# Kernel tuning notes

Measured on AMD Instinct MI355X. Metric: run time of the kernel, lower is better.

Reference implementation:

```python
import jax, jax.numpy as jnp
import numpy as np

D_IN = 4097   # 4096 obj feat + 1 depth
D_H1 = 512
D_H2 = 256
N_HEADS = 4
D_HEAD = D_H2 // N_HEADS
D_FF = 512


def setup_inputs() -> dict:
    key = jax.random.key(0)
    ks = jax.random.split(key, 20)
    B, T, N = 2, 100, 30
    s = lambda *sh: 1.0 / np.sqrt(sh[0])
    inp = {
        "object_features": jax.random.normal(ks[0], (B, T, N, 4096), jnp.float32),
        "object_depths": jax.random.uniform(ks[1], (B, T, N, 1), jnp.float32),
        # spatial encoder (2-layer fully-connected message passing)
        "W1a": jax.random.normal(ks[2], (D_IN, D_H1), jnp.float32) * s(D_IN),
        "W2a": jax.random.normal(ks[3], (D_IN, D_H1), jnp.float32) * s(D_IN),
        "b1a": jnp.zeros((D_H1,), jnp.float32),
        "W1b": jax.random.normal(ks[4], (D_H1, D_H2), jnp.float32) * s(D_H1),
        "W2b": jax.random.normal(ks[5], (D_H1, D_H2), jnp.float32) * s(D_H1),
        "b1b": jnp.zeros((D_H2,), jnp.float32),
        # temporal transformer encoder layer (post-LN)
        "Wq": jax.random.normal(ks[6], (D_H2, D_H2), jnp.float32) * s(D_H2),
        "Wk": jax.random.normal(ks[7], (D_H2, D_H2), jnp.float32) * s(D_H2),
        "Wv": jax.random.normal(ks[8], (D_H2, D_H2), jnp.float32) * s(D_H2),
        "Wo": jax.random.normal(ks[9], (D_H2, D_H2), jnp.float32) * s(D_H2),
        "ln1_g": jnp.ones((D_H2,), jnp.float32),
        "ln1_b": jnp.zeros((D_H2,), jnp.float32),
        "Wf1": jax.random.normal(ks[10], (D_H2, D_FF), jnp.float32) * s(D_H2),
        "bf1": jnp.zeros((D_FF,), jnp.float32),
        "Wf2": jax.random.normal(ks[11], (D_FF, D_H2), jnp.float32) * s(D_FF),
        "bf2": jnp.zeros((D_H2,), jnp.float32),
        "ln2_g": jnp.ones((D_H2,), jnp.float32),
        "ln2_b": jnp.zeros((D_H2,), jnp.float32),
        # classifier
        "Wc": jax.random.normal(ks[12], (D_H2, 1), jnp.float32) * s(D_H2),
        "bc": jnp.zeros((1,), jnp.float32),
    }
    return inp


def _layer_norm(x, g, b, eps=1e-5):
    mu = jnp.mean(x, axis=-1, keepdims=True)
    var = jnp.var(x, axis=-1, keepdims=True)
    return (x - mu) * jax.lax.rsqrt(var + eps) * g + b


def _forward(object_features, object_depths, W1a, W2a, b1a, W1b, W2b, b1b,
             Wq, Wk, Wv, Wo, ln1_g, ln1_b, Wf1, bf1, Wf2, bf2, ln2_g, ln2_b,
             Wc, bc):
    B, T, N, _ = object_features.shape
    x = jnp.concatenate([object_features, object_depths], axis=-1)  # (B,T,N,4097)
    # fully-connected graph (torch.combinations, both directions):
    # aggregated message for node i = mean over all j != i.
    def mp(h, Ws, Wn, b):
        neigh = (jnp.sum(h, axis=2, keepdims=True) - h) / (N - 1)
        return jax.nn.relu(h @ Ws + neigh @ Wn + b)
    h = mp(x, W1a, W2a, b1a)      # (B,T,N,512)
    h = mp(h, W1b, W2b, b1b)      # (B,T,N,256)
    g = jnp.mean(h, axis=2)       # global mean pool -> (B,T,256)
    # temporal transformer encoder (self-attention over T, post-LN)
    q = (g @ Wq).reshape(B, T, N_HEADS, D_HEAD)
    k = (g @ Wk).reshape(B, T, N_HEADS, D_HEAD)
    v = (g @ Wv).reshape(B, T, N_HEADS, D_HEAD)
    scores = jnp.einsum("bthd,bshd->bhts", q, k) / np.sqrt(D_HEAD)
    attn = jax.nn.softmax(scores, axis=-1)
    ctx = jnp.einsum("bhts,bshd->bthd", attn, v).reshape(B, T, D_H2) @ Wo
    y = _layer_norm(g + ctx, ln1_g, ln1_b)
    ff = jax.nn.relu(y @ Wf1 + bf1) @ Wf2 + bf2
    z = _layer_norm(y + ff, ln2_g, ln2_b)  # (B,T,256)
    # dropout is identity in eval mode -> probs2 == probs, uncertainty == 0
    logits = (z @ Wc + bc).squeeze(-1)     # (B,T)
    probs = jax.nn.sigmoid(logits)
    uncertainty = jnp.zeros_like(probs)
    return probs, uncertainty


def reference(object_features, object_depths, W1a, W2a, b1a, W1b, W2b, b1b,
              Wq, Wk, Wv, Wo, ln1_g, ln1_b, Wf1, bf1, Wf2, bf2, ln2_g, ln2_b,
              Wc, bc):
    return _forward(object_features, object_depths, W1a, W2a, b1a, W1b, W2b,
                    b1b, Wq, Wk, Wv, Wo, ln1_g, ln1_b, Wf1, bf1, Wf2, bf2,
                    ln2_g, ln2_b, Wc, bc)
```

## Files before the change

### kernel.cpp

```cpp
#include <hip/hip_runtime.h>
#include <hip/hip_bf16.h>
#include <stdint.h>

typedef unsigned short u16;
typedef __attribute__((ext_vector_type(8))) short short8;
typedef __attribute__((ext_vector_type(4))) float floatx4;
typedef __attribute__((ext_vector_type(4))) unsigned short ushort4_t;

#define BT 200
#define NOBJ 30
#define KP2 4224
#define DIN 4097
#define DH1 512
#define DH2 256
#define DFF 512
#define MPAD 6016
#define CHZ 176
#define NBIGW (132*16)
#define NSMALL 512
#define NCONV (BT*2)
#define NPAD 13
#define NZERO 16

#define PSTR1 ((size_t)6000 * DH1)
#define PSTR2 ((size_t)6000 * DH2)

__device__ __forceinline__ u16 f2bf(float f) {
    union { float f; uint32_t u; } c; c.f = f;
    uint32_t u = c.u;
    u += 0x7FFF + ((u >> 16) & 1);
    return (u16)(u >> 16);
}

__device__ __forceinline__ void load16_lds(const u16* g, u16* l) {
    __builtin_amdgcn_global_load_lds(
        (const __attribute__((address_space(1))) void*)g,
        (__attribute__((address_space(3))) void*)l, 16, 0, 0);
}

__device__ __forceinline__ size_t tile_off(int ytile, int row, int c8) {
    int z = c8 / CHZ, rem = c8 - z * CHZ;
    int i = rem >> 3, kw = rem & 7;
    int ks = kw ^ (row & 7);
    return ((((size_t)(ytile * 3 + z) * 22 + i) * 128 + row) * 64) + ks * 8;
}

__global__ __launch_bounds__(256, 4)
void prep_all(const float* __restrict__ W1a, const float* __restrict__ W2a,
              const float* __restrict__ W1b, const float* __restrict__ W2b,
              const float* __restrict__ feat, const float* __restrict__ depth,
              u16* __restrict__ Wc1T, u16* __restrict__ W2aTs,
              u16* __restrict__ Wc2T, u16* __restrict__ W2bTs,
              u16* __restrict__ XbT, u16* __restrict__ SbT,
              float* __restrict__ zeroBase, size_t zeroQuads) {
    __shared__ float t1[32][33];
    __shared__ float t2[32][33];
    int bid = blockIdx.x, tid = threadIdx.x;
    if (bid < NCONV) {
        int bt = bid >> 1;
        int c8 = ((bid & 1) << 8) + tid;
        int k8 = c8 * 8;
        int zc = c8 / CHZ, rem = c8 - zc * CHZ;
        int ic = rem >> 3, kwc = rem & 7;
        const float* fb = feat + (size_t)bt * NOBJ * 4096 + k8;
        float s[8] = {};
        #pragma unroll 1
        for (int n0 = 0; n0 < NOBJ; n0 += 10) {
            float4 va[10], vb[10];
            #pragma unroll
            for (int u = 0; u < 10; u++) {
                const float* p = fb + (size_t)(n0 + u) * 4096;
                va[u] = *(const float4*)p;
                vb[u] = *(const float4*)(p + 4);
            }
            #pragma unroll
            for (int u = 0; u < 10; u++) {
                int r = bt * NOBJ + n0 + u;
                float v[8] = {va[u].x, va[u].y, va[u].z, va[u].w,
                              vb[u].x, vb[u].y, vb[u].z, vb[u].w};
                short8 o;
                #pragma unroll
                for (int e = 0; e < 8; e++) { s[e] += v[e]; o[e] = (short)f2bf(v[e]); }
                size_t off = ((((size_t)((r >> 7) * 3 + zc) * 22 + ic) * 128
                               + (r & 127)) * 64) + (size_t)(kwc ^ (r & 7)) * 8;
                *(short8*)(XbT + off) = o;
            }
        }
        short8 so;
        #pragma unroll
        for (int e = 0; e < 8; e++) so[e] = (short)f2bf(s[e]);
        {
            int r = bt;
            size_t off = ((((size_t)((r >> 7) * 3 + zc) * 22 + ic) * 128
                           + (r & 127)) * 64) + (size_t)(kwc ^ (r & 7)) * 8;
            *(short8*)(SbT + off) = so;
        }
    } else if (bid < NCONV + NPAD) {
        int idx = (bid - NCONV) * 256 + tid;
        if (idx < 3200) {
            int bt = idx >> 4;
            int c8 = 512 + (idx & 15);
            int rem = c8 - 2 * CHZ;
            int ic = rem >> 3, kwc = rem & 7;
            bool isd = (c8 == 512);
            float dsum = 0.f;
            for (int n = 0; n < NOBJ; n++) {
                int r = bt * NOBJ + n;
                short8 o = {};
                if (isd) { float d = depth[r]; dsum += d; o[0] = (short)f2bf(d); }
                size_t off = ((((size_t)((r >> 7) * 3 + 2) * 22 + ic) * 128
                               + (r & 127)) * 64) + (size_t)(kwc ^ (r & 7)) * 8;
                *(short8*)(XbT + off) = o;
            }
            short8 so = {};
            if (isd) so[0] = (short)f2bf(dsum);
            int r = bt;
            size_t off = ((((size_t)((r >> 7) * 3 + 2) * 22 + ic) * 128
                           + (r & 127)) * 64) + (size_t)(kwc ^ (r & 7)) * 8;
            *(short8*)(SbT + off) = so;
        }
    } else if (bid < NCONV + NPAD + NZERO) {
        int zid = bid - NCONV - NPAD;
        float4* p = (float4*)zeroBase;
        float4 zz = {0.f, 0.f, 0.f, 0.f};
        for (size_t idx = (size_t)zid * 256 + tid; idx < zeroQuads; idx += (size_t)NZERO * 256)
            p[idx] = zz;
    } else if (bid < NCONV + NPAD + NZERO + NSMALL) {
        int idx = (bid - NCONV - NPAD - NZERO) * 256 + tid;
        int j = idx >> 9, k = idx & 511;
        float a = W1b[k * DH2 + j];
        float b = W2b[k * DH2 + j] * (1.f / 29.f);
        Wc2T[j * DH1 + k]  = f2bf(a - b);
        W2bTs[j * DH1 + k] = f2bf(b);
    } else {
        int b2 = bid - NCONV - NPAD - NZERO - NSMALL;
        int kb = (b2 % 132) * 32, jb = (b2 / 132) * 32;
        int tx = tid & 31, ty = tid >> 5;
        #pragma unroll
        for (int r = 0; r < 32; r += 8) {
            int k = kb + ty + r, j = jb + tx;
            float a = 0.f, b = 0.f;
            if (k < DIN) { a = W1a[k * DH1 + j]; b = W2a[k * DH1 + j]; }
            float bs = b * (1.f / 29.f);
            t1[ty + r][tx] = a - bs;
            t2[ty + r][tx] = bs;
        }
        __syncthreads();
        #pragma unroll
        for (int r = 0; r < 32; r += 8) {
            int j = jb + ty + r, k = kb + tx;
            int x = j >> 7, row = j & 127;
            size_t off = tile_off(x, row, k >> 3) + (k & 7);
            Wc1T[off]  = f2bf(t1[tx][ty + r]);
            W2aTs[off] = f2bf(t2[tx][ty + r]);
        }
    }
}

__global__ __launch_bounds__(256) void gemmA(
    const u16* __restrict__ XbT, const u16* __restrict__ WaT,
    const u16* __restrict__ SbT, const u16* __restrict__ WsT,
    float* __restrict__ haccP, float* __restrict__ uOut) {
    __shared__ __align__(16) u16 Al[8192];
    __shared__ __align__(16) u16 Bl[8192];
    int bid = blockIdx.x;
    const u16 *Abase, *Bbase;
    float* outF;
    int m0, n0, M;
    bool useAtomic;
    if (bid < 564) {
        int xcd = bid & 7, slot = bid >> 3;
        int lid = (xcd < 4 ? xcd * 71 : 284 + (xcd - 4) * 70) + slot;
        int x = lid & 3, y = (lid >> 2) % 47, z = lid / 188;
        Abase = XbT + (size_t)((y * 3 + z) * 22) * 8192;
        Bbase = WaT + (size_t)((x * 3 + z) * 22) * 8192;
        outF = haccP + (size_t)z * PSTR1;
        M = 6000; m0 = y * 128; n0 = x * 128; useAtomic = false;
    } else {
        int rem = bid - 564;
        int x = rem & 3, y = (rem >> 2) & 1, z = rem >> 3;
        Abase = SbT + (size_t)((y * 3 + z) * 22) * 8192;
        Bbase = WsT + (size_t)((x * 3 + z) * 22) * 8192;
        outF = uOut; M = BT; m0 = y * 128; n0 = x * 128; useAtomic = true;
    }
    int tid = threadIdx.x, lane = tid & 63, w = tid >> 6;
    floatx4 acc[4][4] = {};
    int lrow = lane & 15, q = lane >> 4;
    int wm = (w & 1) * 64, wn = (w >> 1) * 64;
    int swz = lrow & 7;

    for (int i = 0; i < 22; i++) {
        const u16* as = Abase + (size_t)i * 8192;
        const u16* bs = Bbase + (size_t)i * 8192;
        #pragma unroll
        for (int it = 0; it < 4; it++) {
            load16_lds(as + (it * 256 + tid) * 8, Al + it * 2048 + w * 512);
            load16_lds(bs + (it * 256 + tid) * 8, Bl + it * 2048 + w * 512);
        }
        __syncthreads();
        #pragma unroll
        for (int h = 0; h < 2; h++) {
            int ci = h * 4 + q;
            int so = (ci ^ swz) * 8;
            short8 af[4], bfv[4];
            #pragma unroll
            for (int ii = 0; ii < 4; ii++)
                af[ii] = *(short8*)(Al + (wm + ii * 16 + lrow) * 64 + so);
            #pragma unroll
            for (int j = 0; j < 4; j++)
                bfv[j] = *(short8*)(Bl + (wn + j * 16 + lrow) * 64 + so);
            #pragma unroll
            for (int ii = 0; ii < 4; ii++)
                #pragma unroll
                for (int j = 0; j < 4; j++)
                    acc[ii][j] = __builtin_amdgcn_mfma_f32_16x16x32_bf16(af[ii], bfv[j], acc[ii][j], 0, 0, 0);
        }
        __syncthreads();
    }

    if (useAtomic) {
        #pragma unroll
        for (int ii = 0; ii < 4; ii++)
            #pragma unroll
            for (int j = 0; j < 4; j++)
                #pragma unroll
                for (int r = 0; r < 4; r++) {
                    int row = m0 + wm + ii * 16 + q * 4 + r;
                    int col = n0 + wn + j * 16 + lrow;
                    if (row < M)
                        atomicAdd(&outF[(size_t)row * DH1 + col], acc[ii][j][r]);
                }
    } else {
        #pragma unroll
        for (int ii = 0; ii < 4; ii++)
            #pragma unroll
            for (int j = 0; j < 4; j++)
                #pragma unroll
                for (int r = 0; r < 4; r++) {
                    int row = m0 + wm + ii * 16 + q * 4 + r;
                    int col = n0 + wn + j * 16 + lrow;
                    if (row < M)
                        outF[(size_t)row * DH1 + col] = acc[ii][j][r];
                }
    }
}

__global__ __launch_bounds__(256) void gemmB(
    const u16* __restrict__ hb, const u16* __restrict__ Wc2T,
    const u16* __restrict__ Shb, const u16* __restrict__ W2bTs,
    float* __restrict__ hacc2P, float* __restrict__ u2Out) {
    __shared__ __align__(16) u16 Al[64 * 64];
    __shared__ __align__(16) u16 Bl[128 * 64];
    int bid = blockIdx.x;
    const u16 *A, *B;
    float* outF;
    int m0, n0, kbeg, M;
    bool useAtomic;
    if (bid < 376) {
        int xcd = bid & 7, slot = bid >> 3;
        int lid = xcd * 47 + slot;
        int x = lid & 1, y = (lid >> 1) % 94, z = lid / 188;
        A = hb; B = Wc2T; M = 6000;
        outF = hacc2P + (size_t)z * PSTR2;
        m0 = y * 64; n0 = x * 128; kbeg = z * 256; useAtomic = false;
    } else {
        int rem = bid - 376;
        int x = rem & 1, y = (rem >> 1) & 3, z = rem >> 3;
        A = Shb; B = W2bTs; outF = u2Out; M = BT;
        m0 = y * 64; n0 = x * 128; kbeg = z * 256; useAtomic = true;
    }
    int kend = kbeg + 256;
    const int N = DH2, K = DH1;
    int tid = threadIdx.x;
    int lane = tid & 63, w = tid >> 6;
    int srow = tid >> 3, kslot = tid & 7;
    floatx4 acc[2][4] = {};
    int lrow = lane & 15, q = lane >> 4;
    int wm = (w & 1) * 32, wn = (w >> 1) * 64;
    int swz = lrow & 7;

    for (int kb = kbeg; kb < kend; kb += 64) {
        #pragma unroll
        for (int it = 0; it < 2; it++) {
            int row = it * 32 + srow;
            int kph = kslot ^ (row & 7);
            load16_lds(A + (size_t)(m0 + row) * K + kb + kph * 8,
                       Al + it * 2048 + w * 512);
        }
        #pragma unroll
        for (int it = 0; it < 4; it++) {
            int row = it * 32 + srow;
            int kph = kslot ^ (row & 7);
            load16_lds(B + (size_t)(n0 + row) * K + kb + kph * 8,
                       Bl + it * 2048 + w * 512);
        }
        __syncthreads();
        #pragma unroll
        for (int h = 0; h < 2; h++) {
            int ci = h * 4 + q;
            int so = (ci ^ swz) * 8;
            short8 af[2], bfv[4];
            #pragma unroll
            for (int i = 0; i < 2; i++)
                af[i] = *(short8*)(Al + (wm + i * 16 + lrow) * 64 + so);
            #pragma unroll
            for (int j = 0; j < 4; j++)
                bfv[j] = *(short8*)(Bl + (wn + j * 16 + lrow) * 64 + so);
            #pragma unroll
            for (int i = 0; i < 2; i++)
                #pragma unroll
                for (int j = 0; j < 4; j++)
                    acc[i][j] = __builtin_amdgcn_mfma_f32_16x16x32_bf16(af[i], bfv[j], acc[i][j], 0, 0, 0);
        }
        __syncthreads();
    }

    if (useAtomic) {
        #pragma unroll
        for (int i = 0; i < 2; i++)
            #pragma unroll
            for (int j = 0; j < 4; j++)
                #pragma unroll
                for (int r = 0; r < 4; r++) {
                    int row = m0 + wm + i * 16 + q * 4 + r;
                    int col = n0 + wn + j * 16 + lrow;
                    if (row < M)
                        atomicAdd(&outF[(size_t)row * N + col], acc[i][j][r]);
                }
    } else {
        #pragma unroll
        for (int i = 0; i < 2; i++)
            #pragma unroll
            for (int j = 0; j < 4; j++)
                #pragma unroll
                for (int r = 0; r < 4; r++) {
                    int row = m0 + wm + i * 16 + q * 4 + r;
                    int col = n0 + wn + j * 16 + lrow;
                    if (row < M)
                        outF[(size_t)row * N + col] = acc[i][j][r];
                }
    }
}

__global__ void reduce1(const float* __restrict__ haccP, const float* __restrict__ u,
                        const float* __restrict__ b1a,
                        u16* __restrict__ hb, u16* __restrict__ Shb) {
    __shared__ float sl[128];
    int bt = blockIdx.x, c0 = blockIdx.y * 128;
    int lc = threadIdx.x & 127, rp = threadIdx.x >> 7;
    int col = c0 + lc;
    float ub = u[bt * DH1 + col] + b1a[col];
    float s = 0.f;
    for (int n = rp; n < NOBJ; n += 2) {
        size_t idx = (size_t)(bt * NOBJ + n) * DH1 + col;
        float v = haccP[idx] + haccP[idx + PSTR1] + haccP[idx + 2 * PSTR1] + ub;
        v = v > 0.f ? v : 0.f;
        hb[idx] = f2bf(v);
        s += v;
    }
    if (rp == 0) sl[lc] = s;
    __syncthreads();
    if (rp == 1) Shb[bt * DH1 + col] = f2bf(sl[lc] + s);
}

__global__ void reduce2_qkv(const float* __restrict__ hacc2P, const float* __restrict__ u2,
                            const float* __restrict__ b1b,
                            const float* __restrict__ Wq, const float* __restrict__ Wk,
                            const float* __restrict__ Wv,
                            float* __restrict__ g, float* __restrict__ q,
                            float* __restrict__ k, float* __restrict__ v) {
    __shared__ float gl[DH2];
    int bt = blockIdx.x, j = threadIdx.x;
    float ub = u2[bt * DH2 + j] + b1b[j];
    float a = 0.f;
    for (int n = 0; n < NOBJ; n++) {
        size_t idx = (size_t)(bt * NOBJ + n) * DH2 + j;
        float vv = hacc2P[idx] + hacc2P[idx + PSTR2] + ub;
        a += vv > 0.f ? vv : 0.f;
    }
    a *= (1.f / 30.f);
    gl[j] = a;
    g[bt * DH2 + j] = a;
    __syncthreads();
    float aq = 0.f, ak = 0.f, av = 0.f;
    for (int kk = 0; kk < DH2; kk++) {
        float x = gl[kk];
        aq += x * Wq[kk * DH2 + j];
        ak += x * Wk[kk * DH2 + j];
        av += x * Wv[kk * DH2 + j];
    }
    q[bt * DH2 + j] = aq;
    k[bt * DH2 + j] = ak;
    v[bt * DH2 + j] = av;
}

__device__ __forceinline__ float block_sum256(float v, volatile float* red) {
    #pragma unroll
    for (int o = 32; o > 0; o >>= 1) v += __shfl_down(v, o);
    int w = threadIdx.x >> 6;
    __syncthreads();
    if ((threadIdx.x & 63) == 0) red[w] = v;
    __syncthreads();
    return red[0] + red[1] + red[2] + red[3];
}

__global__ void attn_head(const float* __restrict__ qg, const float* __restrict__ kg,
                          const float* __restrict__ vg, const float* __restrict__ g,
                          const float* __restrict__ Wo,
                          const float* __restrict__ ln1g, const float* __restrict__ ln1b,
                          const float* __restrict__ Wf1, const float* __restrict__ bf1,
                          const float* __restrict__ Wf2, const float* __restrict__ bf2,
                          const float* __restrict__ ln2g, const float* __restrict__ ln2b,
                          const float* __restrict__ Wc, const float* __restrict__ bc,
                          float* __restrict__ out) {
    __shared__ float ql[DH2];
    __shared__ float scl[4][128];
    __shared__ float ctxl[DH2];
    __shared__ float yl[DH2];
    __shared__ float ffl[DFF];
    __shared__ float red[4];
    int row = blockIdx.x, tid = threadIdx.x;
    int base = (row >= 100) ? 100 : 0;
    ql[tid] = qg[row * DH2 + tid];
    __syncthreads();

    for (int p = tid; p < 512; p += 256) {
        int h = p >> 7, s = p & 127;
        if (s < 100) {
            const float* kr = kg + (size_t)(base + s) * DH2 + h * 64;
            float a = 0.f;
            #pragma unroll 8
            for (int d = 0; d < 64; d++) a += ql[h * 64 + d] * kr[d];
            scl[h][s] = a * 0.125f;
        }
    }
    __syncthreads();

    {
        int w = tid >> 6, lane = tid & 63;
        int s2 = 64 + lane;
        float a  = scl[w][lane];
        float b2 = (s2 < 100) ? scl[w][s2] : -1e30f;
        float m = fmaxf(a, b2);
        #pragma unroll
        for (int o = 32; o > 0; o >>= 1) m = fmaxf(m, __shfl_down(m, o));
        m = __shfl(m, 0);
        float e1 = __expf(a - m);
        float e2 = (s2 < 100) ? __expf(b2 - m) : 0.f;
        float sm = e1 + e2;
        #pragma unroll
        for (int o = 32; o > 0; o >>= 1) sm += __shfl_down(sm, o);
        sm = __shfl(sm, 0);
        float r = 1.f / sm;
        scl[w][lane] = e1 * r;
        if (s2 < 100) scl[w][s2] = e2 * r;
    }
    __syncthreads();

    {
        int h = tid >> 6;
        float o = 0.f;
        for (int s = 0; s < 100; s++)
            o += scl[h][s] * vg[(size_t)(base + s) * DH2 + tid];
        ctxl[tid] = o;
    }
    __syncthreads();

    float o = 0.f;
    for (int kk = 0; kk < DH2; kk++) o += ctxl[kk] * Wo[kk * DH2 + tid];
    float t = g[row * DH2 + tid] + o;
    float mu  = block_sum256(t, red) * (1.f / DH2);
    float ex2 = block_sum256(t * t, red) * (1.f / DH2);
    float y = (t - mu) * rsqrtf(ex2 - mu * mu + 1e-5f) * ln1g[tid] + ln1b[tid];
    yl[tid] = y;
    __syncthreads();
    for (int jj = tid; jj < DFF; jj += 256) {
        float a = bf1[jj];
        for (int kk = 0; kk < DH2; kk++) a += yl[kk] * Wf1[kk * DFF + jj];
        ffl[jj] = a > 0.f ? a : 0.f;
    }
    __syncthreads();
    float o2 = bf2[tid];
    for (int kk = 0; kk < DFF; kk++) o2 += ffl[kk] * Wf2[kk * DH2 + tid];
    float z0 = y + o2;
    float mu2  = block_sum256(z0, red) * (1.f / DH2);
    float ex22 = block_sum256(z0 * z0, red) * (1.f / DH2);
    float z = (z0 - mu2) * rsqrtf(ex22 - mu2 * mu2 + 1e-5f) * ln2g[tid] + ln2b[tid];
    float logit = block_sum256(z * Wc[tid], red) + bc[0];
    if (tid == 0) {
        out[row]      = 1.f / (1.f + __expf(-logit));
        out[BT + row] = 0.f;
    }
}

extern "C" void kernel_launch(void* const* d_in, const int* in_sizes, int n_in,
                              void* d_out, int out_size, void* d_ws, size_t ws_size,
                              hipStream_t stream) {
    const float* feat  = (const float*)d_in[0];
    const float* depth = (const float*)d_in[1];
    const float* W1a = (const float*)d_in[2];
    const float* W2a = (const float*)d_in[3];
    const float* b1a = (const float*)d_in[4];
    const float* W1b = (const float*)d_in[5];
    const float* W2b = (const float*)d_in[6];
    const float* b1b = (const float*)d_in[7];
    const float* Wq  = (const float*)d_in[8];
    const float* Wk  = (const float*)d_in[9];
    const float* Wv  = (const float*)d_in[10];
    const float* Wo  = (const float*)d_in[11];
    const float* ln1g = (const float*)d_in[12];
    const float* ln1b = (const float*)d_in[13];
    const float* Wf1 = (const float*)d_in[14];
    const float* bf1 = (const float*)d_in[15];
    const float* Wf2 = (const float*)d_in[16];
    const float* bf2 = (const float*)d_in[17];
    const float* ln2g = (const float*)d_in[18];
    const float* ln2b = (const float*)d_in[19];
    const float* Wc  = (const float*)d_in[20];
    const float* bc  = (const float*)d_in[21];
    float* out = (float*)d_out;
    char* ws = (char*)d_ws;

    size_t off = 0;
    u16* XbT   = (u16*)(ws + off); off += (size_t)MPAD * KP2 * 2;
    u16* SbT   = (u16*)(ws + off); off += (size_t)256 * KP2 * 2;
    u16* Wc1T  = (u16*)(ws + off); off += (size_t)DH1 * KP2 * 2;
    u16* W2aTs = (u16*)(ws + off); off += (size_t)DH1 * KP2 * 2;
    u16* Wc2T  = (u16*)(ws + off); off += (size_t)DH2 * DH1 * 2;
    u16* W2bTs = (u16*)(ws + off); off += (size_t)DH2 * DH1 * 2;
    u16* Shb   = (u16*)(ws + off); off += (size_t)256 * DH1 * 2;
    char* zBase = ws + off;
    float* u     = (float*)(ws + off); off += (size_t)BT * DH1 * 4;
    float* u2    = (float*)(ws + off); off += (size_t)BT * DH2 * 4;
    size_t zeroQuads = (size_t)(ws + off - zBase) / 16;
    float* haccP  = (float*)(ws + off); off += 3 * PSTR1 * 4;
    float* hacc2P = haccP;
    u16* hb = XbT;
    float* g = (float*)SbT;
    float* q = g + BT * DH2;
    float* k = q + BT * DH2;
    float* v = k + BT * DH2;

    prep_all<<<NCONV + NPAD + NZERO + NSMALL + NBIGW, 256, 0, stream>>>(
        W1a, W2a, W1b, W2b, feat, depth,
        Wc1T, W2aTs, Wc2T, W2bTs, XbT, SbT, (float*)zBase, zeroQuads);
    gemmA<<<564 + 24, 256, 0, stream>>>(XbT, Wc1T, SbT, W2aTs, haccP, u);
    reduce1<<<dim3(BT, 4), 256, 0, stream>>>(haccP, u, b1a, hb, Shb);
    gemmB<<<376 + 16, 256, 0, stream>>>(hb, Wc2T, Shb, W2bTs, hacc2P, u2);
    reduce2_qkv<<<BT, DH2, 0, stream>>>(hacc2P, u2, b1b, Wq, Wk, Wv, g, q, k, v);
    attn_head<<<BT, DH2, 0, stream>>>(q, k, v, g, Wo, ln1g, ln1b, Wf1, bf1,
                                      Wf2, bf2, ln2g, ln2b, Wc, bc, out);
}
```

Before: 354.7 us.

## Move temporal transformer matmuls onto bf16 MFMA tile kernels

The per-row scalar QKV, Wo and FFN matmuls are replaced by a generic bf16 MFMA tile GEMM (mm_tail) with fused epilogues for bias, residual and ReLU. Attention and the two layer norms become separate small kernels. The transformer weights are transposed and converted to bf16 inside the existing prep kernel. This removes per-block reloading of full fp32 weight matrices, but adds five kernel launches, extra workspace round-trips and bf16 rounding in the tail.

```diff
diff --git a/kernel.cpp b/kernel.cpp
--- a/kernel.cpp
+++ b/kernel.cpp
@@ -5,7 +5,6 @@
 typedef unsigned short u16;
 typedef __attribute__((ext_vector_type(8))) short short8;
 typedef __attribute__((ext_vector_type(4))) float floatx4;
-typedef __attribute__((ext_vector_type(4))) unsigned short ushort4_t;
 
 #define BT 200
 #define NOBJ 30
@@ -21,6 +20,7 @@
 #define NCONV (BT*2)
 #define NPAD 13
 #define NZERO 16
+#define NTR 512
 
 #define PSTR1 ((size_t)6000 * DH1)
 #define PSTR2 ((size_t)6000 * DH2)
@@ -49,9 +49,14 @@
 void prep_all(const float* __restrict__ W1a, const float* __restrict__ W2a,
               const float* __restrict__ W1b, const float* __restrict__ W2b,
               const float* __restrict__ feat, const float* __restrict__ depth,
+              const float* __restrict__ Wq, const float* __restrict__ Wk,
+              const float* __restrict__ Wv, const float* __restrict__ Wo,
+              const float* __restrict__ Wf1, const float* __restrict__ Wf2,
               u16* __restrict__ Wc1T, u16* __restrict__ W2aTs,
               u16* __restrict__ Wc2T, u16* __restrict__ W2bTs,
               u16* __restrict__ XbT, u16* __restrict__ SbT,
+              u16* __restrict__ qkvT, u16* __restrict__ WoT,
+              u16* __restrict__ Wf1T, u16* __restrict__ Wf2T,
               float* __restrict__ zeroBase, size_t zeroQuads) {
     __shared__ float t1[32][33];
     __shared__ float t2[32][33];
@@ -132,7 +137,7 @@
         float b = W2b[k * DH2 + j] * (1.f / 29.f);
         Wc2T[j * DH1 + k]  = f2bf(a - b);
         W2bTs[j * DH1 + k] = f2bf(b);
-    } else {
+    } else if (bid < NCONV + NPAD + NZERO + NSMALL + NBIGW) {
         int b2 = bid - NCONV - NPAD - NZERO - NSMALL;
         int kb = (b2 % 132) * 32, jb = (b2 / 132) * 32;
         int tx = tid & 31, ty = tid >> 5;
@@ -154,6 +159,36 @@
             Wc1T[off]  = f2bf(t1[tx][ty + r]);
             W2aTs[off] = f2bf(t2[tx][ty + r]);
         }
+    } else {
+        int id = bid - NCONV - NPAD - NZERO - NSMALL - NBIGW;
+        const float* src; u16* dst;
+        int jt, kt, NS, KS;
+        if (id < 192) {
+            int mat = id / 64, rem = id % 64;
+            jt = rem & 7; kt = rem >> 3; NS = 256; KS = 256;
+            src = (mat == 0) ? Wq : (mat == 1 ? Wk : Wv);
+            dst = qkvT + (size_t)mat * 256 * 256;
+        } else if (id < 256) {
+            int rem = id - 192;
+            jt = rem & 7; kt = rem >> 3; NS = 256; KS = 256;
+            src = Wo; dst = WoT;
+        } else if (id < 384) {
+            int rem = id - 256;
+            jt = rem & 15; kt = rem >> 4; NS = 512; KS = 256;
+            src = Wf1; dst = Wf1T;
+        } else {
+            int rem = id - 384;
+            jt = rem & 7; kt = rem >> 3; NS = 256; KS = 512;
+            src = Wf2; dst = Wf2T;
+        }
+        int tx = tid & 31, ty = tid >> 5;
+        #pragma unroll
+        for (int r = 0; r < 32; r += 8)
+            t1[ty + r][tx] = src[(size_t)(kt * 32 + ty + r) * NS + jt * 32 + tx];
+        __syncthreads();
+        #pragma unroll
+        for (int r = 0; r < 32; r += 8)
+            dst[(size_t)(jt * 32 + ty + r) * KS + kt * 32 + tx] = f2bf(t1[tx][ty + r]);
     }
 }
 
@@ -218,31 +253,19 @@
         __syncthreads();
     }
 
-    if (useAtomic) {
-        #pragma unroll
-        for (int ii = 0; ii < 4; ii++)
-            #pragma unroll
-            for (int j = 0; j < 4; j++)
-                #pragma unroll
-                for (int r = 0; r < 4; r++) {
-                    int row = m0 + wm + ii * 16 + q * 4 + r;
-                    int col = n0 + wn + j * 16 + lrow;
-                    if (row < M)
-                        atomicAdd(&outF[(size_t)row * DH1 + col], acc[ii][j][r]);
+    #pragma unroll
+    for (int ii = 0; ii < 4; ii++)
+        #pragma unroll
+        for (int j = 0; j < 4; j++)
+            #pragma unroll
+            for (int r = 0; r < 4; r++) {
+                int row = m0 + wm + ii * 16 + q * 4 + r;
+                int col = n0 + wn + j * 16 + lrow;
+                if (row < M) {
+                    if (useAtomic) atomicAdd(&outF[(size_t)row * DH1 + col], acc[ii][j][r]);
+                    else outF[(size_t)row * DH1 + col] = acc[ii][j][r];
                 }
-    } else {
-        #pragma unroll
-        for (int ii = 0; ii < 4; ii++)
-            #pragma unroll
-            for (int j = 0; j < 4; j++)
-                #pragma unroll
-                for (int r = 0; r < 4; r++) {
-                    int row = m0 + wm + ii * 16 + q * 4 + r;
-                    int col = n0 + wn + j * 16 + lrow;
-                    if (row < M)
-                        outF[(size_t)row * DH1 + col] = acc[ii][j][r];
-                }
-    }
+            }
 }
 
 __global__ __launch_bounds__(256) void gemmB(
@@ -315,31 +338,95 @@
         __syncthreads();
     }
 
-    if (useAtomic) {
-        #pragma unroll
-        for (int i = 0; i < 2; i++)
+    #pragma unroll
+    for (int i = 0; i < 2; i++)
+        #pragma unroll
+        for (int j = 0; j < 4; j++)
+            #pragma unroll
+            for (int r = 0; r < 4; r++) {
+                int row = m0 + wm + i * 16 + q * 4 + r;
+                int col = n0 + wn + j * 16 + lrow;
+                if (row < M) {
+                    if (useAtomic) atomicAdd(&outF[(size_t)row * N + col], acc[i][j][r]);
+                    else outF[(size_t)row * N + col] = acc[i][j][r];
+                }
+            }
+}
+
+__global__ __launch_bounds__(256) void mm_tail(
+    const u16* __restrict__ A, const u16* __restrict__ B,
+    int K, int NT, int ldo,
+    float* __restrict__ outf, u16* __restrict__ outb,
+    const float* __restrict__ addf, const float* __restrict__ bias,
+    int mode) {
+    __shared__ __align__(16) u16 Al[64 * 64];
+    __shared__ __align__(16) u16 Bl[128 * 64];
+    int bid = blockIdx.x;
+    int mt = bid / NT, nt = bid % NT;
+    int m0 = mt * 64, n0 = nt * 128;
+    int tid = threadIdx.x;
+    int lane = tid & 63, w = tid >> 6;
+    int srow = tid >> 3, kslot = tid & 7;
+    floatx4 acc[2][4] = {};
+    int lrow = lane & 15, q = lane >> 4;
+    int wm = (w & 1) * 32, wn = (w >> 1) * 64;
+    int swz = lrow & 7;
+
+    for (int kb = 0; kb < K; kb += 64) {
+        #pragma unroll
+        for (int it = 0; it < 2; it++) {
+            int row = it * 32 + srow;
+            int kph = kslot ^ (row & 7);
+            load16_lds(A + (size_t)(m0 + row) * K + kb + kph * 8,
+                       Al + it * 2048 + w * 512);
+        }
+        #pragma unroll
+        for (int it = 0; it < 4; it++) {
+            int row = it * 32 + srow;
+            int kph = kslot ^ (row & 7);
+            load16_lds(B + (size_t)(n0 + row) * K + kb + kph * 8,
+                       Bl + it * 2048 + w * 512);
+        }
+        __syncthreads();
+        #pragma unroll
+        for (int h = 0; h < 2; h++) {
+            int ci = h * 4 + q;
+            int so = (ci ^ swz) * 8;
+            short8 af[2], bfv[4];
+            #pragma unroll
+            for (int i = 0; i < 2; i++)
+                af[i] = *(short8*)(Al + (wm + i * 16 + lrow) * 64 + so);
             #pragma unroll
             for (int j = 0; j < 4; j++)
+                bfv[j] = *(short8*)(Bl + (wn + j * 16 + lrow) * 64 + so);
+            #pragma unroll
+            for (int i = 0; i < 2; i++)
                 #pragma unroll
-                for (int r = 0; r < 4; r++) {
-                    int row = m0 + wm + i * 16 + q * 4 + r;
-                    int col = n0 + wn + j * 16 + lrow;
-                    if (row < M)
-                        atomicAdd(&outF[(size_t)row * N + col], acc[i][j][r]);
+                for (int j = 0; j < 4; j++)
+                    acc[i][j] = __builtin_amdgcn_mfma_f32_16x16x32_bf16(af[i], bfv[j], acc[i][j], 0, 0, 0);
+        }
+        __syncthreads();
+    }
+
+    #pragma unroll
+    for (int i = 0; i < 2; i++)
+        #pragma unroll
+        for (int j = 0; j < 4; j++)
+            #pragma unroll
+            for (int r = 0; r < 4; r++) {
+                int row = m0 + wm + i * 16 + q * 4 + r;
+                int col = n0 + wn + j * 16 + lrow;
+                if (row < BT) {
+                    float v = acc[i][j][r];
+                    size_t o = (size_t)row * ldo + col;
+                    if (mode == 0) outf[o] = v;
+                    else if (mode == 1) outf[o] = v + addf[o];
+                    else if (mode == 2) {
+                        v += bias[col];
+                        outb[o] = f2bf(v > 0.f ? v : 0.f);
+                    } else outf[o] = v + bias[col] + addf[o];
                 }
-    } else {
-        #pragma unroll
-        for (int i = 0; i < 2; i++)
-            #pragma unroll
-            for (int j = 0; j < 4; j++)
-                #pragma unroll
-                for (int r = 0; r < 4; r++) {
-                    int row = m0 + wm + i * 16 + q * 4 + r;
-                    int col = n0 + wn + j * 16 + lrow;
-                    if (row < M)
-                        outF[(size_t)row * N + col] = acc[i][j][r];
-                }
-    }
+            }
 }
 
 __global__ void reduce1(const float* __restrict__ haccP, const float* __restrict__ u,
@@ -363,13 +450,9 @@
     if (rp == 1) Shb[bt * DH1 + col] = f2bf(sl[lc] + s);
 }
 
-__global__ void reduce2_qkv(const float* __restrict__ hacc2P, const float* __restrict__ u2,
-                            const float* __restrict__ b1b,
-                            const float* __restrict__ Wq, const float* __restrict__ Wk,
-                            const float* __restrict__ Wv,
-                            float* __restrict__ g, float* __restrict__ q,
-                            float* __restrict__ k, float* __restrict__ v) {
-    __shared__ float gl[DH2];
+__global__ void reduce2_g(const float* __restrict__ hacc2P, const float* __restrict__ u2,
+                          const float* __restrict__ b1b,
+                          float* __restrict__ g, u16* __restrict__ gb) {
     int bt = blockIdx.x, j = threadIdx.x;
     float ub = u2[bt * DH2 + j] + b1b[j];
     float a = 0.f;
@@ -379,19 +462,58 @@
         a += vv > 0.f ? vv : 0.f;
     }
     a *= (1.f / 30.f);
-    gl[j] = a;
     g[bt * DH2 + j] = a;
+    gb[bt * DH2 + j] = f2bf(a);
+}
+
+__global__ void attn_ctx(const float* __restrict__ qkv, u16* __restrict__ cb) {
+    __shared__ float ql[DH2];
+    __shared__ float scl[4][128];
+    int row = blockIdx.x, tid = threadIdx.x;
+    int base = (row >= 100) ? 100 : 0;
+    ql[tid] = qkv[(size_t)row * 768 + tid];
     __syncthreads();
-    float aq = 0.f, ak = 0.f, av = 0.f;
-    for (int kk = 0; kk < DH2; kk++) {
-        float x = gl[kk];
-        aq += x * Wq[kk * DH2 + j];
-        ak += x * Wk[kk * DH2 + j];
-        av += x * Wv[kk * DH2 + j];
-    }
-    q[bt * DH2 + j] = aq;
-    k[bt * DH2 + j] = ak;
-    v[bt * DH2 + j] = av;
+
+    for (int p = tid; p < 512; p += 256) {
+        int h = p >> 7, s = p & 127;
+        if (s < 100) {
+            const float* kr = qkv + (size_t)(base + s) * 768 + 256 + h * 64;
+            float a = 0.f;
+            #pragma unroll 8
+            for (int d = 0; d < 64; d++) a += ql[h * 64 + d] * kr[d];
+            scl[h][s] = a * 0.125f;
+        }
+    }
+    __syncthreads();
+
+    {
+        int w = tid >> 6, lane = tid & 63;
+        int s2 = 64 + lane;
+        float a  = scl[w][lane];
+        float b2 = (s2 < 100) ? scl[w][s2] : -1e30f;
+        float m = fmaxf(a, b2);
+        #pragma unroll
+        for (int o = 32; o > 0; o >>= 1) m = fmaxf(m, __shfl_down(m, o));
+        m = __shfl(m, 0);
+        float e1 = __expf(a - m);
+        float e2 = (s2 < 100) ? __expf(b2 - m) : 0.f;
+        float sm = e1 + e2;
+        #pragma unroll
+        for (int o = 32; o > 0; o >>= 1) sm += __shfl_down(sm, o);
+        sm = __shfl(sm, 0);
+        float r = 1.f / sm;
+        scl[w][lane] = e1 * r;
+        if (s2 < 100) scl[w][s2] = e2 * r;
+    }
+    __syncthreads();
+
+    {
+        int h = tid >> 6;
+        float o = 0.f;
+        for (int s = 0; s < 100; s++)
+            o += scl[h][s] * qkv[(size_t)(base + s) * 768 + 512 + tid];
+        cb[(size_t)row * DH2 + tid] = f2bf(o);
+    }
 }
 
 __device__ __forceinline__ float block_sum256(float v, volatile float* red) {
@@ -404,92 +526,32 @@
     return red[0] + red[1] + red[2] + red[3];
 }
 
-__global__ void attn_head(const float* __restrict__ qg, const float* __restrict__ kg,
-                          const float* __restrict__ vg, const float* __restrict__ g,
-                          const float* __restrict__ Wo,
-                          const float* __restrict__ ln1g, const float* __restrict__ ln1b,
-                          const float* __restrict__ Wf1, const float* __restrict__ bf1,
-                          const float* __restrict__ Wf2, const float* __restrict__ bf2,
-                          const float* __restrict__ ln2g, const float* __restrict__ ln2b,
-                          const float* __restrict__ Wc, const float* __restrict__ bc,
-                          float* __restrict__ out) {
-    __shared__ float ql[DH2];
-    __shared__ float scl[4][128];
-    __shared__ float ctxl[DH2];
-    __shared__ float yl[DH2];
-    __shared__ float ffl[DFF];
+__global__ void ln_y(const float* __restrict__ t, const float* __restrict__ ln1g,
+                     const float* __restrict__ ln1b,
+                     float* __restrict__ yf, u16* __restrict__ yb) {
     __shared__ float red[4];
     int row = blockIdx.x, tid = threadIdx.x;
-    int base = (row >= 100) ? 100 : 0;
-    ql[tid] = qg[row * DH2 + tid];
-    __syncthreads();
-
-    for (int p = tid; p < 512; p += 256) {
-        int h = p >> 7, s = p & 127;
-        if (s < 100) {
-            const float* kr = kg + (size_t)(base + s) * DH2 + h * 64;
-            float a = 0.f;
-            #pragma unroll 8
-            for (int d = 0; d < 64; d++) a += ql[h * 64 + d] * kr[d];
-            scl[h][s] = a * 0.125f;
-        }
-    }
-    __syncthreads();
-
-    {
-        int w = tid >> 6, lane = tid & 63;
-        int s2 = 64 + lane;
-        float a  = scl[w][lane];
-        float b2 = (s2 < 100) ? scl[w][s2] : -1e30f;
-        float m = fmaxf(a, b2);
-        #pragma unroll
-        for (int o = 32; o > 0; o >>= 1) m = fmaxf(m, __shfl_down(m, o));
-        m = __shfl(m, 0);
-        float e1 = __expf(a - m);
-        float e2 = (s2 < 100) ? __expf(b2 - m) : 0.f;
-        float sm = e1 + e2;
-        #pragma unroll
-        for (int o = 32; o > 0; o >>= 1) sm += __shfl_down(sm, o);
-        sm = __shfl(sm, 0);
-        float r = 1.f / sm;
-        scl[w][lane] = e1 * r;
-        if (s2 < 100) scl[w][s2] = e2 * r;
-    }
-    __syncthreads();
-
-    {
-        int h = tid >> 6;
-        float o = 0.f;
-        for (int s = 0; s < 100; s++)
-            o += scl[h][s] * vg[(size_t)(base + s) * DH2 + tid];
-        ctxl[tid] = o;
-    }
-    __syncthreads();
-
-    float o = 0.f;
-    for (int kk = 0; kk < DH2; kk++) o += ctxl[kk] * Wo[kk * DH2 + tid];
-    float t = g[row * DH2 + tid] + o;
-    float mu  = block_sum256(t, red) * (1.f / DH2);
-    float ex2 = block_sum256(t * t, red) * (1.f / DH2);
-    float y = (t - mu) * rsqrtf(ex2 - mu * mu + 1e-5f) * ln1g[tid] + ln1b[tid];
-    yl[tid] = y;
-    __syncthreads();
-    for (int jj = tid; jj < DFF; jj += 256) {
-        float a = bf1[jj];
-        for (int kk = 0; kk < DH2; kk++) a += yl[kk] * Wf1[kk * DFF + jj];
-        ffl[jj] = a > 0.f ? a : 0.f;
-    }
-    __syncthreads();
-    float o2 = bf2[tid];
-    for (int kk = 0; kk < DFF; kk++) o2 += ffl[kk] * Wf2[kk * DH2 + tid];
-    float z0 = y + o2;
-    float mu2  = block_sum256(z0, red) * (1.f / DH2);
-    float ex22 = block_sum256(z0 * z0, red) * (1.f / DH2);
-    float z = (z0 - mu2) * rsqrtf(ex22 - mu2 * mu2 + 1e-5f) * ln2g[tid] + ln2b[tid];
+    float tv = t[(size_t)row * DH2 + tid];
+    float mu  = block_sum256(tv, red) * (1.f / DH2);
+    float ex2 = block_sum256(tv * tv, red) * (1.f / DH2);
+    float y = (tv - mu) * rsqrtf(ex2 - mu * mu + 1e-5f) * ln1g[tid] + ln1b[tid];
+    yf[(size_t)row * DH2 + tid] = y;
+    yb[(size_t)row * DH2 + tid] = f2bf(y);
+}
+
+__global__ void ln2_cls(const float* __restrict__ z0, const float* __restrict__ ln2g,
+                        const float* __restrict__ ln2b, const float* __restrict__ Wc,
+                        const float* __restrict__ bc, float* __restrict__ outP) {
+    __shared__ float red[4];
+    int row = blockIdx.x, tid = threadIdx.x;
+    float zv = z0[(size_t)row * DH2 + tid];
+    float mu  = block_sum256(zv, red) * (1.f / DH2);
+    float ex2 = block_sum256(zv * zv, red) * (1.f / DH2);
+    float z = (zv - mu) * rsqrtf(ex2 - mu * mu + 1e-5f) * ln2g[tid] + ln2b[tid];
     float logit = block_sum256(z * Wc[tid], red) + bc[0];
     if (tid == 0) {
-        out[row]      = 1.f / (1.f + __expf(-logit));
-        out[BT + row] = 0.f;
+        outP[row]      = 1.f / (1.f + __expf(-logit));
+        outP[BT + row] = 0.f;
     }
 }
 
@@ -535,19 +597,34 @@
     size_t zeroQuads = (size_t)(ws + off - zBase) / 16;
     float* haccP  = (float*)(ws + off); off += 3 * PSTR1 * 4;
     float* hacc2P = haccP;
+    u16* qkvT = (u16*)(ws + off); off += (size_t)768 * 256 * 2;
+    u16* WoT  = (u16*)(ws + off); off += (size_t)256 * 256 * 2;
+    u16* Wf1T = (u16*)(ws + off); off += (size_t)512 * 256 * 2;
+    u16* Wf2T = (u16*)(ws + off); off += (size_t)256 * 512 * 2;
+    u16* gb   = (u16*)(ws + off); off += (size_t)256 * 256 * 2;
+    u16* cb   = (u16*)(ws + off); off += (size_t)256 * 256 * 2;
+    u16* yb   = (u16*)(ws + off); off += (size_t)256 * 256 * 2;
+    u16* ffb  = (u16*)(ws + off); off += (size_t)256 * 512 * 2;
+    float* qkv = (float*)(ws + off); off += (size_t)BT * 768 * 4;
+    float* t   = (float*)(ws + off); off += (size_t)BT * 256 * 4;
+    float* yf  = (float*)(ws + off); off += (size_t)BT * 256 * 4;
+    float* z0  = (float*)(ws + off); off += (size_t)BT * 256 * 4;
     u16* hb = XbT;
     float* g = (float*)SbT;
-    float* q = g + BT * DH2;
-    float* k = q + BT * DH2;
-    float* v = k + BT * DH2;
-
-    prep_all<<<NCONV + NPAD + NZERO + NSMALL + NBIGW, 256, 0, stream>>>(
-        W1a, W2a, W1b, W2b, feat, depth,
-        Wc1T, W2aTs, Wc2T, W2bTs, XbT, SbT, (float*)zBase, zeroQuads);
+
+    prep_all<<<NCONV + NPAD + NZERO + NSMALL + NBIGW + NTR, 256, 0, stream>>>(
+        W1a, W2a, W1b, W2b, feat, depth, Wq, Wk, Wv, Wo, Wf1, Wf2,
+        Wc1T, W2aTs, Wc2T, W2bTs, XbT, SbT,
+        qkvT, WoT, Wf1T, Wf2T, (float*)zBase, zeroQuads);
     gemmA<<<564 + 24, 256, 0, stream>>>(XbT, Wc1T, SbT, W2aTs, haccP, u);
     reduce1<<<dim3(BT, 4), 256, 0, stream>>>(haccP, u, b1a, hb, Shb);
     gemmB<<<376 + 16, 256, 0, stream>>>(hb, Wc2T, Shb, W2bTs, hacc2P, u2);
-    reduce2_qkv<<<BT, DH2, 0, stream>>>(hacc2P, u2, b1b, Wq, Wk, Wv, g, q, k, v);
-    attn_head<<<BT, DH2, 0, stream>>>(q, k, v, g, Wo, ln1g, ln1b, Wf1, bf1,
-                                      Wf2, bf2, ln2g, ln2b, Wc, bc, out);
-}
+    reduce2_g<<<BT, DH2, 0, stream>>>(hacc2P, u2, b1b, g, gb);
+    mm_tail<<<4 * 6, 256, 0, stream>>>(gb, qkvT, 256, 6, 768, qkv, nullptr, nullptr, nullptr, 0);
+    attn_ctx<<<BT, DH2, 0, stream>>>(qkv, cb);
+    mm_tail<<<4 * 2, 256, 0, stream>>>(cb, WoT, 256, 2, 256, t, nullptr, g, nullptr, 1);
+    ln_y<<<BT, DH2, 0, stream>>>(t, ln1g, ln1b, yf, yb);
+    mm_tail<<<4 * 4, 256, 0, stream>>>(yb, Wf1T, 256, 4, 512, nullptr, ffb, nullptr, bf1, 2);
+    mm_tail<<<4 * 2, 256, 0, stream>>>(ffb, Wf2T, 512, 2, 256, z0, nullptr, yf, bf2, 3);
+    ln2_cls<<<BT, DH2, 0, stream>>>(z0, ln2g, ln2b, Wc, bc, out);
+}
```

Result: faster. 345.8 us (-2.5%).
